# Kernel tuning notes

Hardware: AMD Instinct MI355X
Metric: run time of the kernel (lower is better)

## Reference

```python
import jax, jax.numpy as jnp
import numpy as np
from jax import lax

EPS = 1e-5


def _dcn_core(value, offset, mask, offset_scale):
    # value: (B,H,W,G,D); offset: (B,H,W,G,K,2) as (dx,dy); mask: (B,H,W,G,K)
    # DCNv4: no softmax on mask; sampling loc = center + (kernel_grid + offset)*offset_scale
    B, H, W, G, D = value.shape
    K = mask.shape[-1]
    P = H * W
    kr = jnp.arange(3, dtype=value.dtype) - 1.0
    gy, gx = jnp.meshgrid(kr, kr, indexing="ij")  # 3x3 kernel grid
    gx = gx.reshape(1, 1, 1, 1, K)
    gy = gy.reshape(1, 1, 1, 1, K)
    bx = jnp.arange(W, dtype=value.dtype).reshape(1, 1, W, 1, 1)
    by = jnp.arange(H, dtype=value.dtype).reshape(1, H, 1, 1, 1)
    ix = bx + (gx + offset[..., 0]) * offset_scale  # (B,H,W,G,K) pixel-index coords
    iy = by + (gy + offset[..., 1]) * offset_scale

    tog = lambda a: a.transpose(0, 3, 1, 2, 4).reshape(B, G, P, K)
    ix, iy, m = tog(ix), tog(iy), tog(mask)
    vflat = value.transpose(0, 3, 1, 2, 4).reshape(B, G, P, D)

    x0 = jnp.floor(ix)
    y0 = jnp.floor(iy)
    tx = ix - x0
    ty = iy - y0
    out = jnp.zeros((B, G, P, D), value.dtype)
    # bilinear with zero padding (grid_sample padding_mode='zeros', align_corners=False)
    for dy, dx, wgt in ((0, 0, (1 - ty) * (1 - tx)), (0, 1, (1 - ty) * tx),
                        (1, 0, ty * (1 - tx)), (1, 1, ty * tx)):
        xc = x0 + dx
        yc = y0 + dy
        valid = ((xc >= 0) & (xc < W) & (yc >= 0) & (yc < H)).astype(value.dtype)
        lin = (jnp.clip(yc, 0, H - 1) * W + jnp.clip(xc, 0, W - 1)).astype(jnp.int32)
        v = jnp.take_along_axis(vflat, lin.reshape(B, G, P * K, 1), axis=2)
        v = v.reshape(B, G, P, K, D)
        out = out + jnp.einsum("bgpk,bgpkd->bgpd", wgt * m * valid, v)
    return out.transpose(0, 2, 1, 3).reshape(B, P, G * D)


def setup_inputs() -> dict:
    key = jax.random.key(0)
    ks = jax.random.split(key, 6)
    C = 64
    r = lambda k, shp, s: jax.random.normal(k, shp, jnp.float32) * s
    return {
        "x": r(ks[0], (8, C, 128, 128), 1.0),
        "vp_w": r(ks[1], (C, C), C ** -0.5),
        "vp_b": jnp.zeros((C,), jnp.float32),
        "dw_w": r(ks[2], (C, 1, 3, 3), 1.0 / 3.0),
        "dw_b": jnp.zeros((C,), jnp.float32),
        "om_w": r(ks[3], (56, C), 0.01),
        "om_b": jnp.zeros((56,), jnp.float32),
        "op_w": r(ks[4], (C, C), C ** -0.5),
        "op_b": jnp.zeros((C,), jnp.float32),
        "bn_g": jnp.ones((C // 2,), jnp.float32),
        "bn_b": jnp.zeros((C // 2,), jnp.float32),
        "bn_m": jnp.zeros((C // 2,), jnp.float32),
        "bn_v": jnp.ones((C // 2,), jnp.float32),
    }


def reference(x, vp_w, vp_b, dw_w, dw_b, om_w, om_b, op_w, op_b, bn_g, bn_b, bn_m, bn_v):
    B, C, H, W = x.shape
    G, K, OS = 2, 9, 2.0  # group = in_planes//out_planes = 2; 3x3 -> K=9
    seq = x.reshape(B, H * W, C)  # raw reshape exactly as the torch code
    # DCNv4 value_proj
    val = seq @ vp_w.T + vp_b
    value = val.reshape(B, H, W, G, C // G)
    # offset/mask branch: depthwise 3x3 conv on raw input, then linear
    xi = seq.reshape(B, H, W, C).transpose(0, 3, 1, 2)  # (B,C,H,W)
    dw = lax.conv_general_dilated(xi, dw_w, (1, 1), "SAME",
                                  dimension_numbers=("NCHW", "OIHW", "NCHW"),
                                  feature_group_count=C)
    dw = dw + dw_b[None, :, None, None]
    om = dw.transpose(0, 2, 3, 1) @ om_w.T + om_b  # (B,H,W,56)
    om = om[..., : G * K * 3].reshape(B, H, W, G, 3 * K)  # drop pad-to-8 tail
    offset = om[..., : 2 * K].reshape(B, H, W, G, K, 2)
    mask = om[..., 2 * K:]
    core = _dcn_core(value, offset, mask, OS)  # (B, HW, C)
    out = (core @ op_w.T + op_b).reshape(B, C, H, W)  # raw reshape, as in torch code
    z = 0.5 * (out[:, : C // 2] + out[:, C // 2:])  # chunk + average
    z = bn_g[:, None, None] * (z - bn_m[:, None, None]) * lax.rsqrt(bn_v + EPS)[:, None, None] + bn_b[:, None, None]
    return jnp.maximum(z, 0.0)
```

## Files before the change

### kernel.cpp

```cpp
#include <hip/hip_runtime.h>

#define B_ 8
#define H_ 128
#define W_ 128
#define P_ 16384
#define C_ 64
#define NQ (B_*P_)

typedef _Float16 fp16;
typedef _Float16 half4v __attribute__((ext_vector_type(4)));

static __device__ __forceinline__ void fma4s(float4& a, float s, const float4& v) {
  a.x += s * v.x; a.y += s * v.y; a.z += s * v.z; a.w += s * v.w;
}
static __device__ __forceinline__ void fma4e(float4& a, const float4& u, const float4& v) {
  a.x += u.x * v.x; a.y += u.y * v.y; a.z += u.z * v.z; a.w += u.w * v.w;
}

__global__ __launch_bounds__(256) void gemm_val_kernel(
    const float* __restrict__ X, const float* __restrict__ W,
    const float* __restrict__ bias, fp16* __restrict__ val) {
  __shared__ __align__(16) float Xs[128][68];
  __shared__ __align__(16) float Ws[64][68];
  int tid = threadIdx.x;
  int bid = blockIdx.x;
  int logical = (bid & 7) * 128 + (bid >> 3);
  size_t row0 = (size_t)logical * 128;

#pragma unroll
  for (int i0 = 0; i0 < 8192; i0 += 1024) {
    int i = i0 + tid * 4;
    int r = i >> 6, k = i & 63;
    *(float4*)&Xs[r][k] = *(const float4*)(X + row0 * 64 + i);
  }
#pragma unroll
  for (int i0 = 0; i0 < 4096; i0 += 1024) {
    int i = i0 + tid * 4;
    int c = i >> 6, k = i & 63;
    float4 wv = *(const float4*)(W + i);
    Ws[k][c] = wv.x; Ws[k + 1][c] = wv.y; Ws[k + 2][c] = wv.z; Ws[k + 3][c] = wv.w;
  }
  __syncthreads();

  int ty = tid >> 4, tx = tid & 15;
  int c0 = tx * 4;
  float4 b4 = *(const float4*)(bias + c0);
  float4 acc[8];
#pragma unroll
  for (int rr = 0; rr < 8; ++rr) acc[rr] = b4;
#pragma unroll 4
  for (int k0 = 0; k0 < 64; k0 += 4) {
    float4 w0 = *(const float4*)&Ws[k0][c0];
    float4 w1 = *(const float4*)&Ws[k0 + 1][c0];
    float4 w2 = *(const float4*)&Ws[k0 + 2][c0];
    float4 w3 = *(const float4*)&Ws[k0 + 3][c0];
#pragma unroll
    for (int rr = 0; rr < 8; ++rr) {
      float4 xv = *(const float4*)&Xs[ty + rr * 16][k0];
      fma4s(acc[rr], xv.x, w0); fma4s(acc[rr], xv.y, w1);
      fma4s(acc[rr], xv.z, w2); fma4s(acc[rr], xv.w, w3);
    }
  }
#pragma unroll
  for (int rr = 0; rr < 8; ++rr) {
    int r = ty + rr * 16;
    half4v hv;
    hv.x = (fp16)acc[rr].x; hv.y = (fp16)acc[rr].y;
    hv.z = (fp16)acc[rr].z; hv.w = (fp16)acc[rr].w;
    *(half4v*)(val + (row0 + r) * 64 + c0) = hv;
  }
}

__global__ __launch_bounds__(256) void dwom_kernel(
    const float* __restrict__ X, const float* __restrict__ dw_w,
    const float* __restrict__ dw_b, const float* __restrict__ om_w,
    const float* __restrict__ om_b, float* __restrict__ OM) {
  __shared__ __align__(16) float dws[128][68];
  __shared__ __align__(16) float omwT[64][60];
  __shared__ __align__(16) float dwwT[9][68];
  __shared__ __align__(16) float dwbs[64];
  __shared__ __align__(16) float ombs[56];
  int tid = threadIdx.x;
  int bid = blockIdx.x;
  int logical = (bid & 7) * 128 + (bid >> 3);
  int q0 = logical * 128;
  int b = q0 >> 14;
  int h = logical & 127;

  for (int i = tid; i < 3456; i += 256) omwT[i & 63][i >> 6] = om_w[i];
  for (int i = tid; i < 576; i += 256) dwwT[i % 9][i / 9] = dw_w[i];
  if (tid < 64) dwbs[tid] = dw_b[tid];
  if (tid < 56) ombs[tid] = (tid < 54) ? om_b[tid] : 0.f;
  __syncthreads();

  {
    int cv = tid & 15;
    int lqq = tid >> 4;
    int c0 = cv * 4;
    const float* xb = X + (size_t)b * 1048576;
    float4 wt[9];
#pragma unroll
    for (int t = 0; t < 9; ++t) wt[t] = *(const float4*)&dwwT[t][c0];
    float4 dwb4 = *(const float4*)&dwbs[c0];
#pragma unroll
    for (int it = 0; it < 8; ++it) {
      int lq = lqq + 16 * it;
      float4 acc = dwb4;
#pragma unroll
      for (int t = 0; t < 9; ++t) {
        int dy = t / 3 - 1, dx = t % 3 - 1;
        int hh = h + dy, wx = lq + dx;
        if ((unsigned)hh < 128u && (unsigned)wx < 128u) {
          float4 v = *(const float4*)(xb + (((size_t)(hh * 128 + wx)) << 6) + c0);
          fma4e(acc, v, wt[t]);
        }
      }
      *(float4*)&dws[lq][c0] = acc;
    }
  }
  __syncthreads();

  int ty = tid >> 4, tx = tid & 15;
  int o0 = tx * 4;
  if (o0 < 54) {
    float4 b4 = *(const float4*)&ombs[o0];
    float4 acc[8];
#pragma unroll
    for (int rr = 0; rr < 8; ++rr) acc[rr] = b4;
#pragma unroll 4
    for (int k0 = 0; k0 < 64; k0 += 4) {
      float4 w0 = *(const float4*)&omwT[k0][o0];
      float4 w1 = *(const float4*)&omwT[k0 + 1][o0];
      float4 w2 = *(const float4*)&omwT[k0 + 2][o0];
      float4 w3 = *(const float4*)&omwT[k0 + 3][o0];
#pragma unroll
      for (int rr = 0; rr < 8; ++rr) {
        float4 dv = *(const float4*)&dws[ty + rr * 16][k0];
        fma4s(acc[rr], dv.x, w0); fma4s(acc[rr], dv.y, w1);
        fma4s(acc[rr], dv.z, w2); fma4s(acc[rr], dv.w, w3);
      }
    }
#pragma unroll
    for (int rr = 0; rr < 8; ++rr) {
      int r = ty + rr * 16;
      size_t base = (size_t)(q0 + r) * 54 + o0;
      if (o0 <= 48) {
        *(float4*)(OM + base) = acc[rr];
      } else {
        *(float2*)(OM + base) = make_float2(acc[rr].x, acc[rr].y);
      }
    }
  }
}

__global__ __launch_bounds__(512, 4) void dcn_fused_kernel(
    const fp16* __restrict__ val, const float* __restrict__ OM,
    const float* __restrict__ op_w, const float* __restrict__ op_b,
    const float* __restrict__ bn_g, const float* __restrict__ bn_b,
    const float* __restrict__ bn_m, const float* __restrict__ bn_v,
    float* __restrict__ out) {
  __shared__ __align__(16) float oms2[128 * 2 * 28];
  __shared__ __align__(16) float cs[128][68];
  __shared__ __align__(16) float Ws[64][68];
  int tid = threadIdx.x;
  int bid = blockIdx.x;
  int logical = (bid & 7) * 128 + (bid >> 3);
  int b = logical >> 7;
  int p0 = (logical & 127) << 6;
  int q0lo = b * 16384 + p0;

#pragma unroll
  for (int i0 = 0; i0 < 4096; i0 += 2048) {
    int i = i0 + tid * 4;
    int c = i >> 6, k = i & 63;
    float4 wv = *(const float4*)(op_w + i);
    Ws[k][c] = wv.x; Ws[k + 1][c] = wv.y; Ws[k + 2][c] = wv.z; Ws[k + 3][c] = wv.w;
  }
  {
    const float* srcLo = OM + (size_t)q0lo * 54;
    const float* srcHi = OM + (size_t)(q0lo + 8192) * 54;
    for (int j = tid; j < 6912; j += 512) {
      float v = (j < 3456) ? srcLo[j] : srcHi[j - 3456];
      int row = j / 54;
      int o = j - row * 54;
      int g = o >= 27;
      int oo = o - 27 * g;
      oms2[(row * 2 + g) * 28 + oo] = v;
    }
  }
  __syncthreads();

  {
    int lq = tid >> 4;
    int g = (tid >> 3) & 1;
    int dv = tid & 7;
    const fp16* vbase = val + ((size_t)b << 20) + g * 32 + dv * 4;
#pragma unroll
    for (int t = 0; t < 4; ++t) {
      int row = lq + 32 * t;
      int hi = row >> 6;
      int w = (p0 & 127) + (row & 63);
      int h = (p0 >> 7) + (hi << 6);
      const float* og = oms2 + (row * 2 + g) * 28;
      float fw = (float)w, fh = (float)h;
      float4 acc = make_float4(0.f, 0.f, 0.f, 0.f);
#pragma unroll
      for (int k = 0; k < 9; ++k) {
        float2 oxy = *(const float2*)(og + 2 * k);
        float m = og[18 + k];
        float ix = fw + ((float)(k % 3) - 1.0f + oxy.x) * 2.0f;
        float iy = fh + ((float)(k / 3) - 1.0f + oxy.y) * 2.0f;
        float x0f = floorf(ix), y0f = floorf(iy);
        float tx = ix - x0f, ty = iy - y0f;
        int x0 = (int)x0f, y0 = (int)y0f;
        int x1 = x0 + 1, y1 = y0 + 1;
        float vx0 = ((unsigned)x0 < 128u) ? 1.f : 0.f;
        float vx1 = ((unsigned)x1 < 128u) ? 1.f : 0.f;
        float vy0 = ((unsigned)y0 < 128u) ? 1.f : 0.f;
        float vy1 = ((unsigned)y1 < 128u) ? 1.f : 0.f;
        int xc0 = min(max(x0, 0), 127), xc1 = min(max(x1, 0), 127);
        int yc0 = min(max(y0, 0), 127), yc1 = min(max(y1, 0), 127);
        float w00 = (1.f - ty) * (1.f - tx) * m * vy0 * vx0;
        float w01 = (1.f - ty) * tx * m * vy0 * vx1;
        float w10 = ty * (1.f - tx) * m * vy1 * vx0;
        float w11 = ty * tx * m * vy1 * vx1;
        half4v v00 = *(const half4v*)(vbase + ((size_t)((yc0 * 128 + xc0)) << 6));
        half4v v01 = *(const half4v*)(vbase + ((size_t)((yc0 * 128 + xc1)) << 6));
        half4v v10 = *(const half4v*)(vbase + ((size_t)((yc1 * 128 + xc0)) << 6));
        half4v v11 = *(const half4v*)(vbase + ((size_t)((yc1 * 128 + xc1)) << 6));
        float4 f00 = {(float)v00.x, (float)v00.y, (float)v00.z, (float)v00.w};
        float4 f01 = {(float)v01.x, (float)v01.y, (float)v01.z, (float)v01.w};
        float4 f10 = {(float)v10.x, (float)v10.y, (float)v10.z, (float)v10.w};
        float4 f11 = {(float)v11.x, (float)v11.y, (float)v11.z, (float)v11.w};
        fma4s(acc, w00, f00); fma4s(acc, w01, f01);
        fma4s(acc, w10, f10); fma4s(acc, w11, f11);
      }
      *(float4*)&cs[row][g * 32 + dv * 4] = acc;
    }
  }
  __syncthreads();

  int tyg = tid >> 4;
  int txg = tid & 15;
  if (tyg < 16) {
    int c0 = txg * 4;
    float4 accL[4], accH[4];
#pragma unroll
    for (int m = 0; m < 4; ++m) {
      accL[m] = make_float4(0.f, 0.f, 0.f, 0.f);
      accH[m] = make_float4(0.f, 0.f, 0.f, 0.f);
    }
#pragma unroll 2
    for (int k0 = 0; k0 < 64; k0 += 4) {
      float4 w0 = *(const float4*)&Ws[k0][c0];
      float4 w1 = *(const float4*)&Ws[k0 + 1][c0];
      float4 w2 = *(const float4*)&Ws[k0 + 2][c0];
      float4 w3 = *(const float4*)&Ws[k0 + 3][c0];
#pragma unroll
      for (int m = 0; m < 4; ++m) {
        int r = tyg + 16 * m;
        float4 aL = *(const float4*)&cs[r][k0];
        float4 aH = *(const float4*)&cs[r + 64][k0];
        fma4s(accL[m], aL.x, w0); fma4s(accL[m], aL.y, w1);
        fma4s(accL[m], aL.z, w2); fma4s(accL[m], aL.w, w3);
        fma4s(accH[m], aH.x, w0); fma4s(accH[m], aH.y, w1);
        fma4s(accH[m], aH.z, w2); fma4s(accH[m], aH.w, w3);
      }
    }
    float4 bias4 = *(const float4*)(op_b + c0);
#pragma unroll
    for (int m = 0; m < 4; ++m) {
      int r = tyg + 16 * m;
      int f = (p0 + r) * 64 + c0;
      int c2 = f >> 14;
      float scale = bn_g[c2] * rsqrtf(bn_v[c2] + 1e-5f);
      float shift = bn_b[c2] - bn_m[c2] * scale;
      float4 z;
      z.x = fmaxf((0.5f * (accL[m].x + accH[m].x) + bias4.x) * scale + shift, 0.f);
      z.y = fmaxf((0.5f * (accL[m].y + accH[m].y) + bias4.y) * scale + shift, 0.f);
      z.z = fmaxf((0.5f * (accL[m].z + accH[m].z) + bias4.z) * scale + shift, 0.f);
      z.w = fmaxf((0.5f * (accL[m].w + accH[m].w) + bias4.w) * scale + shift, 0.f);
      *(float4*)(out + (size_t)b * 524288 + f) = z;
    }
  }
}

extern "C" void kernel_launch(void* const* d_in, const int* in_sizes, int n_in,
                              void* d_out, int out_size, void* d_ws, size_t ws_size,
                              hipStream_t stream) {
  const float* x    = (const float*)d_in[0];
  const float* vp_w = (const float*)d_in[1];
  const float* vp_b = (const float*)d_in[2];
  const float* dw_w = (const float*)d_in[3];
  const float* dw_b = (const float*)d_in[4];
  const float* om_w = (const float*)d_in[5];
  const float* om_b = (const float*)d_in[6];
  const float* op_w = (const float*)d_in[7];
  const float* op_b = (const float*)d_in[8];
  const float* bn_g = (const float*)d_in[9];
  const float* bn_b = (const float*)d_in[10];
  const float* bn_m = (const float*)d_in[11];
  const float* bn_v = (const float*)d_in[12];

  float* ws   = (float*)d_ws;
  fp16* val_h = (fp16*)d_ws;
  float* om   = ws + 16777216;

  gemm_val_kernel<<<dim3(1024), dim3(256), 0, stream>>>(x, vp_w, vp_b, val_h);
  dwom_kernel<<<dim3(1024), dim3(256), 0, stream>>>(x, dw_w, dw_b, om_w, om_b, om);
  dcn_fused_kernel<<<dim3(1024), dim3(512), 0, stream>>>(
      val_h, om, op_w, op_b, bn_g, bn_b, bn_m, bn_v, (float*)d_out);
}
```

Measured before the change: 136.0 us.

## Split fused DCN kernel into gather and GEMM-BN kernels with fp16 intermediates

Stores the offset/mask tensor in fp16 instead of fp32. The fused sample-plus-projection kernel is split into two: a gather kernel that precomputes bilinear weights and packed corner indices in shared memory and writes the sampled core tensor in fp16, and a separate kernel that runs the output projection GEMM with batch-norm and ReLU. The aim is lower register and shared-memory pressure in the gather, which should allow higher occupancy and better latency hiding for the random gathers. The cost is an extra kernel launch, an extra fp16 round trip of the core tensor through memory, and reduced precision for offsets and core values.

```diff
diff --git a/kernel.cpp b/kernel.cpp
--- a/kernel.cpp
+++ b/kernel.cpp
@@ -8,13 +8,18 @@
 #define NQ (B_*P_)
 
 typedef _Float16 fp16;
+typedef _Float16 half2v __attribute__((ext_vector_type(2)));
 typedef _Float16 half4v __attribute__((ext_vector_type(4)));
+typedef _Float16 half8v __attribute__((ext_vector_type(8)));
 
 static __device__ __forceinline__ void fma4s(float4& a, float s, const float4& v) {
   a.x += s * v.x; a.y += s * v.y; a.z += s * v.z; a.w += s * v.w;
 }
 static __device__ __forceinline__ void fma4e(float4& a, const float4& u, const float4& v) {
   a.x += u.x * v.x; a.y += u.y * v.y; a.z += u.z * v.z; a.w += u.w * v.w;
+}
+static __device__ __forceinline__ float4 h2f(half4v h) {
+  return make_float4((float)h.x, (float)h.y, (float)h.z, (float)h.w);
 }
 
 __global__ __launch_bounds__(256) void gemm_val_kernel(
@@ -74,7 +79,7 @@
 __global__ __launch_bounds__(256) void dwom_kernel(
     const float* __restrict__ X, const float* __restrict__ dw_w,
     const float* __restrict__ dw_b, const float* __restrict__ om_w,
-    const float* __restrict__ om_b, float* __restrict__ OM) {
+    const float* __restrict__ om_b, fp16* __restrict__ OM) {
   __shared__ __align__(16) float dws[128][68];
   __shared__ __align__(16) float omwT[64][60];
   __shared__ __align__(16) float dwwT[9][68];
@@ -145,143 +150,166 @@
       int r = ty + rr * 16;
       size_t base = (size_t)(q0 + r) * 54 + o0;
       if (o0 <= 48) {
-        *(float4*)(OM + base) = acc[rr];
+        half4v hv;
+        hv.x = (fp16)acc[rr].x; hv.y = (fp16)acc[rr].y;
+        hv.z = (fp16)acc[rr].z; hv.w = (fp16)acc[rr].w;
+        *(half4v*)(OM + base) = hv;
       } else {
-        *(float2*)(OM + base) = make_float2(acc[rr].x, acc[rr].y);
+        half2v hv2;
+        hv2.x = (fp16)acc[rr].x; hv2.y = (fp16)acc[rr].y;
+        *(half2v*)(OM + base) = hv2;
       }
     }
   }
 }
 
-__global__ __launch_bounds__(512, 4) void dcn_fused_kernel(
-    const fp16* __restrict__ val, const float* __restrict__ OM,
-    const float* __restrict__ op_w, const float* __restrict__ op_b,
-    const float* __restrict__ bn_g, const float* __restrict__ bn_b,
-    const float* __restrict__ bn_m, const float* __restrict__ bn_v,
-    float* __restrict__ out) {
-  __shared__ __align__(16) float oms2[128 * 2 * 28];
-  __shared__ __align__(16) float cs[128][68];
+__global__ __launch_bounds__(256, 6) void gather_kernel(
+    const fp16* __restrict__ val, const fp16* __restrict__ OM,
+    fp16* __restrict__ core) {
+  __shared__ __align__(16) float4 wtab[64 * 2 * 9];
+  __shared__ int btab[64 * 2 * 9];
+  int tid = threadIdx.x;
+  int bid = blockIdx.x;
+  int logical = (bid & 7) * 256 + (bid >> 3);
+  int b = logical >> 8;
+  int q0 = logical * 64;
+
+  for (int i = tid; i < 1152; i += 256) {
+    int row = i / 18;
+    int rem = i - row * 18;
+    int g = rem / 9;
+    int k = rem - g * 9;
+    int q = q0 + row;
+    int p = q & 16383;
+    int h = p >> 7, w = p & 127;
+    const fp16* omq = OM + (size_t)q * 54 + g * 27;
+    float ox = (float)omq[2 * k], oy = (float)omq[2 * k + 1];
+    float m = (float)omq[18 + k];
+    int kx = k - (k / 3) * 3, ky = k / 3;
+    float ix = (float)w + ((float)kx - 1.0f + ox) * 2.0f;
+    float iy = (float)h + ((float)ky - 1.0f + oy) * 2.0f;
+    float x0f = floorf(ix), y0f = floorf(iy);
+    float tx = ix - x0f, ty = iy - y0f;
+    int x0 = (int)x0f, y0 = (int)y0f;
+    int x1 = x0 + 1, y1 = y0 + 1;
+    float vx0 = ((unsigned)x0 < 128u) ? 1.f : 0.f;
+    float vx1 = ((unsigned)x1 < 128u) ? 1.f : 0.f;
+    float vy0 = ((unsigned)y0 < 128u) ? 1.f : 0.f;
+    float vy1 = ((unsigned)y1 < 128u) ? 1.f : 0.f;
+    int xc0 = min(max(x0, 0), 127), xc1 = min(max(x1, 0), 127);
+    int yc0 = min(max(y0, 0), 127), yc1 = min(max(y1, 0), 127);
+    float4 w4;
+    w4.x = (1.f - ty) * (1.f - tx) * m * vy0 * vx0;
+    w4.y = (1.f - ty) * tx * m * vy0 * vx1;
+    w4.z = ty * (1.f - tx) * m * vy1 * vx0;
+    w4.w = ty * tx * m * vy1 * vx1;
+    wtab[i] = w4;
+    btab[i] = (yc0 * 128 + xc0) | ((xc1 - xc0) << 14) | ((yc1 - yc0) << 15);
+  }
+  __syncthreads();
+
+  int lq = tid >> 4;
+  int g = (tid >> 3) & 1;
+  int dv = tid & 7;
+  const fp16* vbase = val + ((size_t)b << 20) + g * 32 + dv * 4;
+  fp16* cbase = core + (size_t)q0 * 64 + g * 32 + dv * 4;
+  for (int t = 0; t < 4; ++t) {
+    int row = lq + 16 * t;
+    int base = (row * 2 + g) * 9;
+    float4 acc = make_float4(0.f, 0.f, 0.f, 0.f);
+#pragma unroll
+    for (int k = 0; k < 9; ++k) {
+      float4 w4 = wtab[base + k];
+      int pk = btab[base + k];
+      int lin00 = pk & 16383;
+      int dxo = (pk >> 14) & 1;
+      int lin10 = lin00 + ((pk >> 15) << 7);
+      half4v v00 = *(const half4v*)(vbase + ((size_t)lin00 << 6));
+      half4v v01 = *(const half4v*)(vbase + ((size_t)(lin00 + dxo) << 6));
+      half4v v10 = *(const half4v*)(vbase + ((size_t)lin10 << 6));
+      half4v v11 = *(const half4v*)(vbase + ((size_t)(lin10 + dxo) << 6));
+      fma4s(acc, w4.x, h2f(v00));
+      fma4s(acc, w4.y, h2f(v01));
+      fma4s(acc, w4.z, h2f(v10));
+      fma4s(acc, w4.w, h2f(v11));
+    }
+    half4v hv;
+    hv.x = (fp16)acc.x; hv.y = (fp16)acc.y; hv.z = (fp16)acc.z; hv.w = (fp16)acc.w;
+    *(half4v*)(cbase + ((size_t)row << 6)) = hv;
+  }
+}
+
+__global__ __launch_bounds__(256) void gemmbn_kernel(
+    const fp16* __restrict__ core, const float* __restrict__ op_w,
+    const float* __restrict__ op_b, const float* __restrict__ bn_g,
+    const float* __restrict__ bn_b, const float* __restrict__ bn_m,
+    const float* __restrict__ bn_v, float* __restrict__ out) {
   __shared__ __align__(16) float Ws[64][68];
+  __shared__ __align__(16) fp16 csL[64][72];
+  __shared__ __align__(16) fp16 csH[64][72];
   int tid = threadIdx.x;
   int bid = blockIdx.x;
   int logical = (bid & 7) * 128 + (bid >> 3);
   int b = logical >> 7;
-  int p0 = (logical & 127) << 6;
-  int q0lo = b * 16384 + p0;
-
-#pragma unroll
-  for (int i0 = 0; i0 < 4096; i0 += 2048) {
+  int p0 = (logical & 127) * 64;
+  size_t q0lo = (size_t)b * 16384 + p0;
+
+#pragma unroll
+  for (int i0 = 0; i0 < 4096; i0 += 1024) {
     int i = i0 + tid * 4;
     int c = i >> 6, k = i & 63;
     float4 wv = *(const float4*)(op_w + i);
     Ws[k][c] = wv.x; Ws[k + 1][c] = wv.y; Ws[k + 2][c] = wv.z; Ws[k + 3][c] = wv.w;
   }
-  {
-    const float* srcLo = OM + (size_t)q0lo * 54;
-    const float* srcHi = OM + (size_t)(q0lo + 8192) * 54;
-    for (int j = tid; j < 6912; j += 512) {
-      float v = (j < 3456) ? srcLo[j] : srcHi[j - 3456];
-      int row = j / 54;
-      int o = j - row * 54;
-      int g = o >= 27;
-      int oo = o - 27 * g;
-      oms2[(row * 2 + g) * 28 + oo] = v;
-    }
-  }
-  __syncthreads();
-
-  {
-    int lq = tid >> 4;
-    int g = (tid >> 3) & 1;
-    int dv = tid & 7;
-    const fp16* vbase = val + ((size_t)b << 20) + g * 32 + dv * 4;
-#pragma unroll
-    for (int t = 0; t < 4; ++t) {
-      int row = lq + 32 * t;
-      int hi = row >> 6;
-      int w = (p0 & 127) + (row & 63);
-      int h = (p0 >> 7) + (hi << 6);
-      const float* og = oms2 + (row * 2 + g) * 28;
-      float fw = (float)w, fh = (float)h;
-      float4 acc = make_float4(0.f, 0.f, 0.f, 0.f);
-#pragma unroll
-      for (int k = 0; k < 9; ++k) {
-        float2 oxy = *(const float2*)(og + 2 * k);
-        float m = og[18 + k];
-        float ix = fw + ((float)(k % 3) - 1.0f + oxy.x) * 2.0f;
-        float iy = fh + ((float)(k / 3) - 1.0f + oxy.y) * 2.0f;
-        float x0f = floorf(ix), y0f = floorf(iy);
-        float tx = ix - x0f, ty = iy - y0f;
-        int x0 = (int)x0f, y0 = (int)y0f;
-        int x1 = x0 + 1, y1 = y0 + 1;
-        float vx0 = ((unsigned)x0 < 128u) ? 1.f : 0.f;
-        float vx1 = ((unsigned)x1 < 128u) ? 1.f : 0.f;
-        float vy0 = ((unsigned)y0 < 128u) ? 1.f : 0.f;
-        float vy1 = ((unsigned)y1 < 128u) ? 1.f : 0.f;
-        int xc0 = min(max(x0, 0), 127), xc1 = min(max(x1, 0), 127);
-        int yc0 = min(max(y0, 0), 127), yc1 = min(max(y1, 0), 127);
-        float w00 = (1.f - ty) * (1.f - tx) * m * vy0 * vx0;
-        float w01 = (1.f - ty) * tx * m * vy0 * vx1;
-        float w10 = ty * (1.f - tx) * m * vy1 * vx0;
-        float w11 = ty * tx * m * vy1 * vx1;
-        half4v v00 = *(const half4v*)(vbase + ((size_t)((yc0 * 128 + xc0)) << 6));
-        half4v v01 = *(const half4v*)(vbase + ((size_t)((yc0 * 128 + xc1)) << 6));
-        half4v v10 = *(const half4v*)(vbase + ((size_t)((yc1 * 128 + xc0)) << 6));
-        half4v v11 = *(const half4v*)(vbase + ((size_t)((yc1 * 128 + xc1)) << 6));
-        float4 f00 = {(float)v00.x, (float)v00.y, (float)v00.z, (float)v00.w};
-        float4 f01 = {(float)v01.x, (float)v01.y, (float)v01.z, (float)v01.w};
-        float4 f10 = {(float)v10.x, (float)v10.y, (float)v10.z, (float)v10.w};
-        float4 f11 = {(float)v11.x, (float)v11.y, (float)v11.z, (float)v11.w};
-        fma4s(acc, w00, f00); fma4s(acc, w01, f01);
-        fma4s(acc, w10, f10); fma4s(acc, w11, f11);
-      }
-      *(float4*)&cs[row][g * 32 + dv * 4] = acc;
-    }
-  }
-  __syncthreads();
-
-  int tyg = tid >> 4;
-  int txg = tid & 15;
-  if (tyg < 16) {
-    int c0 = txg * 4;
-    float4 accL[4], accH[4];
+#pragma unroll
+  for (int j0 = 0; j0 < 512; j0 += 256) {
+    int j = j0 + tid;
+    int r = j >> 3;
+    int cc = (j & 7) * 8;
+    *(half8v*)&csL[r][cc] = *(const half8v*)(core + (q0lo + r) * 64 + cc);
+    *(half8v*)&csH[r][cc] = *(const half8v*)(core + (q0lo + 8192 + r) * 64 + cc);
+  }
+  __syncthreads();
+
+  int ty = tid >> 4, tx = tid & 15;
+  int c0 = tx * 4;
+  float4 accL[4], accH[4];
+#pragma unroll
+  for (int m = 0; m < 4; ++m) {
+    accL[m] = make_float4(0.f, 0.f, 0.f, 0.f);
+    accH[m] = make_float4(0.f, 0.f, 0.f, 0.f);
+  }
+#pragma unroll 2
+  for (int k0 = 0; k0 < 64; k0 += 4) {
+    float4 w0 = *(const float4*)&Ws[k0][c0];
+    float4 w1 = *(const float4*)&Ws[k0 + 1][c0];
+    float4 w2 = *(const float4*)&Ws[k0 + 2][c0];
+    float4 w3 = *(const float4*)&Ws[k0 + 3][c0];
 #pragma unroll
     for (int m = 0; m < 4; ++m) {
-      accL[m] = make_float4(0.f, 0.f, 0.f, 0.f);
-      accH[m] = make_float4(0.f, 0.f, 0.f, 0.f);
-    }
-#pragma unroll 2
-    for (int k0 = 0; k0 < 64; k0 += 4) {
-      float4 w0 = *(const float4*)&Ws[k0][c0];
-      float4 w1 = *(const float4*)&Ws[k0 + 1][c0];
-      float4 w2 = *(const float4*)&Ws[k0 + 2][c0];
-      float4 w3 = *(const float4*)&Ws[k0 + 3][c0];
-#pragma unroll
-      for (int m = 0; m < 4; ++m) {
-        int r = tyg + 16 * m;
-        float4 aL = *(const float4*)&cs[r][k0];
-        float4 aH = *(const float4*)&cs[r + 64][k0];
-        fma4s(accL[m], aL.x, w0); fma4s(accL[m], aL.y, w1);
-        fma4s(accL[m], aL.z, w2); fma4s(accL[m], aL.w, w3);
-        fma4s(accH[m], aH.x, w0); fma4s(accH[m], aH.y, w1);
-        fma4s(accH[m], aH.z, w2); fma4s(accH[m], aH.w, w3);
-      }
-    }
-    float4 bias4 = *(const float4*)(op_b + c0);
-#pragma unroll
-    for (int m = 0; m < 4; ++m) {
-      int r = tyg + 16 * m;
-      int f = (p0 + r) * 64 + c0;
-      int c2 = f >> 14;
-      float scale = bn_g[c2] * rsqrtf(bn_v[c2] + 1e-5f);
-      float shift = bn_b[c2] - bn_m[c2] * scale;
-      float4 z;
-      z.x = fmaxf((0.5f * (accL[m].x + accH[m].x) + bias4.x) * scale + shift, 0.f);
-      z.y = fmaxf((0.5f * (accL[m].y + accH[m].y) + bias4.y) * scale + shift, 0.f);
-      z.z = fmaxf((0.5f * (accL[m].z + accH[m].z) + bias4.z) * scale + shift, 0.f);
-      z.w = fmaxf((0.5f * (accL[m].w + accH[m].w) + bias4.w) * scale + shift, 0.f);
-      *(float4*)(out + (size_t)b * 524288 + f) = z;
-    }
+      int r = ty + 16 * m;
+      float4 aL = h2f(*(const half4v*)&csL[r][k0]);
+      float4 aH = h2f(*(const half4v*)&csH[r][k0]);
+      fma4s(accL[m], aL.x, w0); fma4s(accL[m], aL.y, w1);
+      fma4s(accL[m], aL.z, w2); fma4s(accL[m], aL.w, w3);
+      fma4s(accH[m], aH.x, w0); fma4s(accH[m], aH.y, w1);
+      fma4s(accH[m], aH.z, w2); fma4s(accH[m], aH.w, w3);
+    }
+  }
+  float4 bias4 = *(const float4*)(op_b + c0);
+#pragma unroll
+  for (int m = 0; m < 4; ++m) {
+    int r = ty + 16 * m;
+    int f = (p0 + r) * 64 + c0;
+    int c2 = f >> 14;
+    float scale = bn_g[c2] * rsqrtf(bn_v[c2] + 1e-5f);
+    float shift = bn_b[c2] - bn_m[c2] * scale;
+    float4 z;
+    z.x = fmaxf((0.5f * (accL[m].x + accH[m].x) + bias4.x) * scale + shift, 0.f);
+    z.y = fmaxf((0.5f * (accL[m].y + accH[m].y) + bias4.y) * scale + shift, 0.f);
+    z.z = fmaxf((0.5f * (accL[m].z + accH[m].z) + bias4.z) * scale + shift, 0.f);
+    z.w = fmaxf((0.5f * (accL[m].w + accH[m].w) + bias4.w) * scale + shift, 0.f);
+    *(float4*)(out + (size_t)b * 524288 + f) = z;
   }
 }
 
@@ -302,12 +330,13 @@
   const float* bn_m = (const float*)d_in[11];
   const float* bn_v = (const float*)d_in[12];
 
-  float* ws   = (float*)d_ws;
-  fp16* val_h = (fp16*)d_ws;
-  float* om   = ws + 16777216;
+  fp16* val_h  = (fp16*)d_ws;
+  fp16* core_h = (fp16*)((char*)d_ws + (16u << 20));
+  fp16* om_h   = (fp16*)((char*)d_ws + (32u << 20));
 
   gemm_val_kernel<<<dim3(1024), dim3(256), 0, stream>>>(x, vp_w, vp_b, val_h);
-  dwom_kernel<<<dim3(1024), dim3(256), 0, stream>>>(x, dw_w, dw_b, om_w, om_b, om);
-  dcn_fused_kernel<<<dim3(1024), dim3(512), 0, stream>>>(
-      val_h, om, op_w, op_b, bn_g, bn_b, bn_m, bn_v, (float*)d_out);
-}
+  dwom_kernel<<<dim3(1024), dim3(256), 0, stream>>>(x, dw_w, dw_b, om_w, om_b, om_h);
+  gather_kernel<<<dim3(2048), dim3(256), 0, stream>>>(val_h, om_h, core_h);
+  gemmbn_kernel<<<dim3(1024), dim3(256), 0, stream>>>(
+      core_h, op_w, op_b, bn_g, bn_b, bn_m, bn_v, (float*)d_out);
+}
```

Result: faster. 127.0 us (-6.7%).
